# Optimization experiments

Hardware: AMD Instinct MI355X
Metric: run time of the kernel (lower is better)

## Reference

```python
import jax, jax.numpy as jnp
import numpy as np

D_MODEL = 1024
NUM_HEAD = 16
D_K = D_MODEL // NUM_HEAD
FFN_D = 4096
EPS = 1e-5


def _layernorm(x, gamma, beta):
    mu = jnp.mean(x, axis=-1, keepdims=True)
    var = jnp.mean(jnp.square(x - mu), axis=-1, keepdims=True)
    return (x - mu) * jax.lax.rsqrt(var + EPS) * gamma + beta


def setup_inputs() -> dict:
    key = jax.random.key(0)
    ks = jax.random.split(key, 16)
    s = 1.0 / np.sqrt(D_MODEL)
    sf = 1.0 / np.sqrt(FFN_D)
    # weights stored as [in, out] (transpose of torch nn.Linear.weight)
    return {
        "x": jax.random.normal(ks[0], (4, 2048, D_MODEL), dtype=jnp.float32),
        "wq": jax.random.uniform(ks[1], (D_MODEL, D_MODEL), jnp.float32, -s, s),
        "bq": jax.random.uniform(ks[2], (D_MODEL,), jnp.float32, -s, s),
        "wk": jax.random.uniform(ks[3], (D_MODEL, D_MODEL), jnp.float32, -s, s),
        "bk": jax.random.uniform(ks[4], (D_MODEL,), jnp.float32, -s, s),
        "wv": jax.random.uniform(ks[5], (D_MODEL, D_MODEL), jnp.float32, -s, s),
        "bv": jax.random.uniform(ks[6], (D_MODEL,), jnp.float32, -s, s),
        "wo": jax.random.uniform(ks[7], (D_MODEL, D_MODEL), jnp.float32, -s, s),
        "bo": jax.random.uniform(ks[8], (D_MODEL,), jnp.float32, -s, s),
        "w1": jax.random.uniform(ks[9], (D_MODEL, FFN_D), jnp.float32, -s, s),
        "b1": jax.random.uniform(ks[10], (FFN_D,), jnp.float32, -s, s),
        "w2": jax.random.uniform(ks[11], (FFN_D, D_MODEL), jnp.float32, -sf, sf),
        "b2": jax.random.uniform(ks[12], (D_MODEL,), jnp.float32, -sf, sf),
        "g1": jnp.ones((D_MODEL,), jnp.float32),
        "be1": jnp.zeros((D_MODEL,), jnp.float32),
        "g2": jnp.ones((D_MODEL,), jnp.float32),
        "be2": jnp.zeros((D_MODEL,), jnp.float32),
    }


def reference(x, wq, bq, wk, bk, wv, bv, wo, bo, w1, b1, w2, b2, g1, be1, g2, be2):
    B, S, _ = x.shape
    resid1 = x
    # project and split heads: [B, H, S, d_k]
    def heads(w, b):
        return (x @ w + b).reshape(B, S, NUM_HEAD, D_K).transpose(0, 2, 1, 3)
    q = heads(wq, bq)
    k = heads(wk, bk)
    v = heads(wv, bv)
    scores = jnp.einsum("bhsd,bhtd->bhst", q, k) / jnp.sqrt(jnp.float32(D_K))
    attn = jax.nn.softmax(scores, axis=-1)
    ctx = jnp.einsum("bhst,bhtd->bhsd", attn, v)
    ctx = ctx.transpose(0, 2, 1, 3).reshape(B, S, D_MODEL)
    attn_out = ctx @ wo + bo
    x1 = _layernorm(resid1 + attn_out, g1, be1)
    ffn = jax.nn.relu(x1 @ w1 + b1) @ w2 + b2
    return _layernorm(x1 + ffn, g2, be2)
```

## Files before the change

### kernel.cpp

```cpp
#include <hip/hip_runtime.h>

typedef unsigned short u16;
typedef __attribute__((ext_vector_type(8))) u16 u16x8;
typedef __attribute__((ext_vector_type(8))) __bf16 bf16x8;
typedef __attribute__((ext_vector_type(4))) float floatx4;
typedef __attribute__((ext_vector_type(16))) float floatx16;
typedef __attribute__((ext_vector_type(4))) unsigned int u32x4;

#define MFMA16(a, b, c) __builtin_amdgcn_mfma_f32_16x16x32_bf16( \
    __builtin_bit_cast(bf16x8, a), __builtin_bit_cast(bf16x8, b), c, 0, 0, 0)
#define MFMA32(a, b, c) __builtin_amdgcn_mfma_f32_32x32x16_bf16( \
    __builtin_bit_cast(bf16x8, a), __builtin_bit_cast(bf16x8, b), c, 0, 0, 0)

#if __has_builtin(__builtin_amdgcn_exp2f)
#define EXP2(x) __builtin_amdgcn_exp2f(x)
#else
#define EXP2(x) exp2f(x)
#endif

__device__ __forceinline__ float bf2f(u16 h) {
  unsigned u = ((unsigned)h) << 16;
  float f;
  __builtin_memcpy(&f, &u, 4);
  return f;
}
__device__ __forceinline__ u16 f2bf(float f) {
  unsigned u;
  __builtin_memcpy(&u, &f, 4);
  u += 0x7fff + ((u >> 16) & 1);
  return (u16)(u >> 16);
}

__device__ __forceinline__ unsigned cvt_pk_bf16(float a, float b) {
  unsigned r;
  asm("v_cvt_pk_bf16_f32 %0, %1, %2" : "=v"(r) : "v"(a), "v"(b));
  return r;
}
__device__ __forceinline__ void pl32_swap(unsigned& a, unsigned& b) {
  asm("v_permlane32_swap_b32 %0, %1" : "+v"(a), "+v"(b));
}

typedef __attribute__((address_space(1))) const unsigned int gas_u32;
typedef __attribute__((address_space(3))) unsigned int las_u32;

__device__ __forceinline__ void gld_lds16(const u16* g, u16* l) {
  __builtin_amdgcn_global_load_lds((gas_u32*)g, (las_u32*)l, 16, 0, 0);
}

__global__ __launch_bounds__(256) void transpose_k(const float* __restrict__ in,
                                                   u16* __restrict__ out, int R, int C) {
  __shared__ u16 tile[64][65];
  int c0 = blockIdx.x * 64, r0 = blockIdx.y * 64;
  int tc = threadIdx.x & 63, tr = threadIdx.x >> 6;
#pragma unroll
  for (int i = 0; i < 16; ++i)
    tile[tr + i * 4][tc] = f2bf(in[(size_t)(r0 + tr + i * 4) * C + c0 + tc]);
  __syncthreads();
#pragma unroll
  for (int i = 0; i < 16; ++i)
    out[(size_t)(c0 + tr + i * 4) * R + r0 + tc] = tile[tc][tr + i * 4];
}

__global__ __launch_bounds__(256) void convert_k(const float* __restrict__ in,
                                                 u16* __restrict__ out) {
  size_t idx = ((size_t)blockIdx.x * 256 + threadIdx.x) * 8;
  floatx4 f0 = *(const floatx4*)(in + idx);
  floatx4 f1 = *(const floatx4*)(in + idx + 4);
  u16x8 o;
#pragma unroll
  for (int e = 0; e < 4; ++e) o[e] = f2bf(f0[e]);
#pragma unroll
  for (int e = 0; e < 4; ++e) o[4 + e] = f2bf(f1[e]);
  *(u16x8*)(out + idx) = o;
}

template <bool C_F32, bool BIAS_ROW>
__global__ __launch_bounds__(256, 2) void gemm_bt(const u16* __restrict__ A,
                                                  const u16* __restrict__ BT,
                                                  const float* __restrict__ bias,
                                                  void* __restrict__ Cv, int M, int N, int K,
                                                  int relu) {
  __shared__ __align__(16) u16 As[128 * 32];
  __shared__ __align__(16) u16 Bs[128 * 32];
  const int tid = threadIdx.x, lane = tid & 63, wave = tid >> 6;
  const int quad = lane >> 4, l15 = lane & 15;
  const int wr = wave >> 1, wc = wave & 1;
  const int m0 = blockIdx.x * 128, n0 = blockIdx.y * 128;

  floatx4 acc[4][4] = {};

  for (int k0 = 0; k0 < K; k0 += 32) {
#pragma unroll
    for (int p = 0; p < 2; ++p) {
      int chunk = p * 256 + tid;
      int row = chunk >> 2, cc = chunk & 3;
      int ldsbase = (p * 256 + wave * 64) * 8;
      gld_lds16(A + (size_t)(m0 + row) * K + k0 + cc * 8, As + ldsbase);
      gld_lds16(BT + (size_t)(n0 + row) * K + k0 + cc * 8, Bs + ldsbase);
    }
    __syncthreads();
    u16x8 af[4], bfr[4];
#pragma unroll
    for (int i = 0; i < 4; ++i)
      af[i] = *(const u16x8*)(As + (wr * 64 + i * 16 + l15) * 32 + quad * 8);
#pragma unroll
    for (int j = 0; j < 4; ++j)
      bfr[j] = *(const u16x8*)(Bs + (wc * 64 + j * 16 + l15) * 32 + quad * 8);
#pragma unroll
    for (int i = 0; i < 4; ++i)
#pragma unroll
      for (int j = 0; j < 4; ++j) acc[i][j] = MFMA16(af[i], bfr[j], acc[i][j]);
    __syncthreads();
  }

#pragma unroll
  for (int j = 0; j < 4; ++j) {
    int col = n0 + wc * 64 + j * 16 + l15;
    float bv = BIAS_ROW ? 0.f : bias[col];
#pragma unroll
    for (int i = 0; i < 4; ++i) {
      int row = m0 + wr * 64 + i * 16 + quad * 4;
#pragma unroll
      for (int r = 0; r < 4; ++r) {
        float v = acc[i][j][r] + (BIAS_ROW ? bias[row + r] : bv);
        if (relu) v = fmaxf(v, 0.f);
        if (C_F32)
          ((float*)Cv)[(size_t)(row + r) * N + col] = v;
        else
          ((u16*)Cv)[(size_t)(row + r) * N + col] = f2bf(v);
      }
    }
  }
}

__global__ __launch_bounds__(256, 4) void attn_k(const u16* __restrict__ Q,
                                                 const u16* __restrict__ Km,
                                                 const u16* __restrict__ Vt,
                                                 u16* __restrict__ O) {
  __shared__ __align__(16) u16 sh[16384];
  const int tid = threadIdx.x, lane = tid & 63, w = tid >> 6;
  const int hi = lane >> 5, l31 = lane & 31;
  const int b = blockIdx.z, h = blockIdx.y, q0 = blockIdx.x * 128;
  const size_t tokbase = (size_t)b * 2048;

#pragma unroll
  for (int p = 0; p < 4; ++p) {
    int chunk = p * 256 + tid, row = chunk >> 3, cc = chunk & 7;
    int gc = cc ^ (row & 7);
    gld_lds16(Q + (tokbase + q0 + row) * 1024 + h * 64 + gc * 8, sh + (p * 256 + w * 64) * 8);
  }
  __syncthreads();
  u16x8 qf[4];
#pragma unroll
  for (int kt = 0; kt < 4; ++kt) {
    int r = w * 32 + l31;
    int sel = (kt * 2 + hi) ^ (r & 7);
    u16x8 t = *(const u16x8*)(sh + r * 64 + sel * 8);
#pragma unroll
    for (int e = 0; e < 8; ++e) t[e] = f2bf(bf2f(t[e]) * 0.18033688011f);
    qf[kt] = t;
  }
  __syncthreads();

  floatx16 oacc0 = {}, oacc1 = {};
  float lsum = 0.f;

  auto stage = [&](int it2, int buf) {
    int t0 = it2 * 64;
#pragma unroll
    for (int p = 0; p < 2; ++p) {
      int chunk = p * 256 + tid;
      int row = chunk >> 3, cc = chunk & 7;
      int gc = cc ^ (row & 7);
      int ldsoff = (p * 256 + w * 64) * 8;
      gld_lds16(Km + (tokbase + t0 + row) * 1024 + h * 64 + gc * 8, sh + buf * 4096 + ldsoff);
      gld_lds16(Vt + ((size_t)(h * 64 + row)) * 8192 + tokbase + t0 + gc * 8,
                sh + 8192 + buf * 4096 + ldsoff);
    }
  };

  stage(0, 0);

  for (int it = 0; it < 32; ++it) {
    const int cur = it & 1;
    __syncthreads();
    if (it + 1 < 32) stage(it + 1, cur ^ 1);
    const u16* kb = sh + cur * 4096;
    const u16* vb = sh + 8192 + cur * 4096;

    u32x4 pf[4];
#pragma unroll
    for (int tt = 0; tt < 2; ++tt) {
      u16x8 ka[4];
#pragma unroll
      for (int kt = 0; kt < 4; ++kt) {
        int r = tt * 32 + l31;
        ka[kt] = *(const u16x8*)(kb + r * 64 + (((kt * 2 + hi) ^ (r & 7)) * 8));
      }
      floatx16 s = {};
      __builtin_amdgcn_s_setprio(1);
#pragma unroll
      for (int kt = 0; kt < 4; ++kt) s = MFMA32(ka[kt], qf[kt], s);
      __builtin_amdgcn_s_setprio(0);

      float p[16];
#pragma unroll
      for (int r = 0; r < 16; ++r) p[r] = EXP2(s[r]);
#pragma unroll
      for (int r = 0; r < 16; ++r) lsum += p[r];
#pragma unroll
      for (int half = 0; half < 2; ++half) {
        unsigned X0 = cvt_pk_bf16(p[half * 8 + 0], p[half * 8 + 1]);
        unsigned X1 = cvt_pk_bf16(p[half * 8 + 2], p[half * 8 + 3]);
        unsigned Y0 = cvt_pk_bf16(p[half * 8 + 4], p[half * 8 + 5]);
        unsigned Y1 = cvt_pk_bf16(p[half * 8 + 6], p[half * 8 + 7]);
        pl32_swap(X0, Y0);
        pl32_swap(X1, Y1);
        u32x4 f;
        f[0] = X0; f[1] = X1; f[2] = Y0; f[3] = Y1;
        pf[tt * 2 + half] = f;
      }
    }

    {
      u16x8 va[4];
#pragma unroll
      for (int kt = 0; kt < 4; ++kt) {
        int r = l31;
        va[kt] = *(const u16x8*)(vb + r * 64 + (((kt * 2 + hi) ^ (r & 7)) * 8));
      }
      __builtin_amdgcn_s_setprio(1);
#pragma unroll
      for (int kt = 0; kt < 4; ++kt)
        oacc0 = MFMA32(va[kt], __builtin_bit_cast(u16x8, pf[kt]), oacc0);
      __builtin_amdgcn_s_setprio(0);
#pragma unroll
      for (int kt = 0; kt < 4; ++kt) {
        int r = 32 + l31;
        va[kt] = *(const u16x8*)(vb + r * 64 + (((kt * 2 + hi) ^ (r & 7)) * 8));
      }
      __builtin_amdgcn_s_setprio(1);
#pragma unroll
      for (int kt = 0; kt < 4; ++kt)
        oacc1 = MFMA32(va[kt], __builtin_bit_cast(u16x8, pf[kt]), oacc1);
      __builtin_amdgcn_s_setprio(0);
    }
  }

  __syncthreads();
  float tot = lsum + __shfl_xor(lsum, 32);
  float inv = 1.0f / fmaxf(tot, 1e-30f);
  const int qrow = w * 32 + l31;
#pragma unroll
  for (int dt = 0; dt < 2; ++dt) {
    const floatx16& oa = dt ? oacc1 : oacc0;
#pragma unroll
    for (int pr = 0; pr < 8; ++pr) {
      float a = oa[2 * pr] * inv, bb = oa[2 * pr + 1] * inv;
      unsigned pkw = (unsigned)f2bf(a) | ((unsigned)f2bf(bb) << 16);
      int d = dt * 32 + (pr & 1) * 2 + (pr >> 1) * 8 + 4 * hi;
      *(unsigned*)(sh + qrow * 72 + d) = pkw;
    }
  }
  __syncthreads();
#pragma unroll
  for (int p2 = 0; p2 < 4; ++p2) {
    int c = p2 * 64 + lane, rl = c >> 3, cc = c & 7;
    u16x8 vv = *(const u16x8*)(sh + (w * 32 + rl) * 72 + cc * 8);
    *(u16x8*)(O + (tokbase + q0 + w * 32 + rl) * 1024 + h * 64 + cc * 8) = vv;
  }
}

template <bool A_F32, bool B_F32, bool OUT_F32>
__global__ __launch_bounds__(256) void ln_k(const void* __restrict__ Av,
                                            const void* __restrict__ Bv,
                                            const float* __restrict__ g,
                                            const float* __restrict__ be,
                                            void* __restrict__ outv) {
  const int lane = threadIdx.x & 63, wave = threadIdx.x >> 6;
  const size_t row = (size_t)blockIdx.x * 4 + wave;
  const size_t base = row * 1024 + lane * 16;
  float v[16];
  if (A_F32) {
    const float* a = (const float*)Av + base;
#pragma unroll
    for (int q = 0; q < 4; ++q) {
      floatx4 t = *(const floatx4*)(a + q * 4);
#pragma unroll
      for (int e = 0; e < 4; ++e) v[q * 4 + e] = t[e];
    }
  } else {
    const u16* a = (const u16*)Av + base;
    u16x8 a0 = *(const u16x8*)a, a1 = *(const u16x8*)(a + 8);
#pragma unroll
    for (int e = 0; e < 8; ++e) {
      v[e] = bf2f(a0[e]);
      v[e + 8] = bf2f(a1[e]);
    }
  }
  if (B_F32) {
    const float* bb = (const float*)Bv + base;
#pragma unroll
    for (int q = 0; q < 4; ++q) {
      floatx4 t = *(const floatx4*)(bb + q * 4);
#pragma unroll
      for (int e = 0; e < 4; ++e) v[q * 4 + e] += t[e];
    }
  } else {
    const u16* bb = (const u16*)Bv + base;
    u16x8 b0 = *(const u16x8*)bb, b1 = *(const u16x8*)(bb + 8);
#pragma unroll
    for (int e = 0; e < 8; ++e) {
      v[e] += bf2f(b0[e]);
      v[e + 8] += bf2f(b1[e]);
    }
  }
  float sum = 0.f, sq = 0.f;
#pragma unroll
  for (int e = 0; e < 16; ++e) {
    sum += v[e];
    sq += v[e] * v[e];
  }
#pragma unroll
  for (int mk = 1; mk < 64; mk <<= 1) {
    sum += __shfl_xor(sum, mk);
    sq += __shfl_xor(sq, mk);
  }
  float mu = sum * (1.f / 1024.f);
  float var = fmaxf(sq * (1.f / 1024.f) - mu * mu, 0.f);
  float rstd = rsqrtf(var + 1e-5f);
  if (OUT_F32) {
    float* o = (float*)outv + base;
#pragma unroll
    for (int q = 0; q < 4; ++q) {
      floatx4 t;
#pragma unroll
      for (int e = 0; e < 4; ++e) {
        int c = lane * 16 + q * 4 + e;
        t[e] = (v[q * 4 + e] - mu) * rstd * g[c] + be[c];
      }
      *(floatx4*)(o + q * 4) = t;
    }
  } else {
    u16x8 o0, o1;
#pragma unroll
    for (int e = 0; e < 8; ++e) {
      int c = lane * 16 + e;
      o0[e] = f2bf((v[e] - mu) * rstd * g[c] + be[c]);
      o1[e] = f2bf((v[e + 8] - mu) * rstd * g[c + 8] + be[c + 8]);
    }
    *(u16x8*)((u16*)outv + base) = o0;
    *(u16x8*)((u16*)outv + base + 8) = o1;
  }
}

extern "C" void kernel_launch(void* const* d_in, const int* in_sizes, int n_in, void* d_out,
                              int out_size, void* d_ws, size_t ws_size, hipStream_t stream) {
  const float* x = (const float*)d_in[0];
  const float* wq = (const float*)d_in[1];
  const float* bq = (const float*)d_in[2];
  const float* wk = (const float*)d_in[3];
  const float* bk = (const float*)d_in[4];
  const float* wv = (const float*)d_in[5];
  const float* bv = (const float*)d_in[6];
  const float* wo = (const float*)d_in[7];
  const float* bo = (const float*)d_in[8];
  const float* w1 = (const float*)d_in[9];
  const float* b1 = (const float*)d_in[10];
  const float* w2 = (const float*)d_in[11];
  const float* b2 = (const float*)d_in[12];
  const float* g1 = (const float*)d_in[13];
  const float* be1 = (const float*)d_in[14];
  const float* g2 = (const float*)d_in[15];
  const float* be2 = (const float*)d_in[16];
  float* out = (float*)d_out;

  u16* W = (u16*)d_ws;
  const size_t M1 = (size_t)1 << 20;
  u16* wqT = W;
  u16* wkT = wqT + M1;
  u16* wvT = wkT + M1;
  u16* woT = wvT + M1;
  u16* w1T = woT + M1;
  u16* w2T = w1T + 4 * M1;
  u16* arena = w2T + 4 * M1;
  const size_t S8M = (size_t)8 << 20;
  u16* xb = arena;
  u16* Qb = arena + S8M;
  u16* Kb = arena + 2 * S8M;
  u16* Vtb = arena + 3 * S8M;
  u16* Cb = arena + 4 * S8M;
  u16* AO = Qb;
  u16* X1 = xb;
  u16* F1 = Qb;

  dim3 blk(256);
  transpose_k<<<dim3(16, 16), blk, 0, stream>>>(wq, wqT, 1024, 1024);
  transpose_k<<<dim3(16, 16), blk, 0, stream>>>(wk, wkT, 1024, 1024);
  transpose_k<<<dim3(16, 16), blk, 0, stream>>>(wv, wvT, 1024, 1024);
  transpose_k<<<dim3(16, 16), blk, 0, stream>>>(wo, woT, 1024, 1024);
  transpose_k<<<dim3(64, 16), blk, 0, stream>>>(w1, w1T, 1024, 4096);
  transpose_k<<<dim3(16, 64), blk, 0, stream>>>(w2, w2T, 4096, 1024);
  convert_k<<<4096, blk, 0, stream>>>(x, xb);

  gemm_bt<false, false><<<dim3(64, 8), blk, 0, stream>>>(xb, wqT, bq, Qb, 8192, 1024, 1024, 0);
  gemm_bt<false, false><<<dim3(64, 8), blk, 0, stream>>>(xb, wkT, bk, Kb, 8192, 1024, 1024, 0);
  gemm_bt<false, true><<<dim3(8, 64), blk, 0, stream>>>(wvT, xb, bv, Vtb, 1024, 8192, 1024, 0);

  attn_k<<<dim3(16, 16, 4), blk, 0, stream>>>(Qb, Kb, Vtb, Cb);

  gemm_bt<false, false><<<dim3(64, 8), blk, 0, stream>>>(Cb, woT, bo, AO, 8192, 1024, 1024, 0);
  ln_k<true, false, false><<<2048, blk, 0, stream>>>(x, AO, g1, be1, X1);

  gemm_bt<false, false><<<dim3(64, 32), blk, 0, stream>>>(X1, w1T, b1, F1, 8192, 4096, 1024, 1);
  gemm_bt<true, false><<<dim3(64, 8), blk, 0, stream>>>(F1, w2T, b2, out, 8192, 1024, 4096, 0);
  ln_k<false, true, true><<<2048, blk, 0, stream>>>(X1, out, g2, be2, out);
}
```

Measured before the change: 575.7 us.

## Double-buffer GEMM LDS tiles with BK=64 and XOR-swizzled layout

The bf16 GEMM kernel now uses two LDS buffers with a 64-wide K tile. The loads for the next tile are issued right after a single barrier, so they overlap the MFMA work on the current tile, and the second barrier per iteration is gone. Tile columns are XOR-swizzled by row to cut LDS bank conflicts on the fragment reads. LDS use per block rises to 64KB, which could limit occupancy, and the barrier's implicit wait on outstanding loads may limit how much overlap is actually achieved.

```diff
diff --git a/kernel.cpp b/kernel.cpp
--- a/kernel.cpp
+++ b/kernel.cpp
@@ -80,8 +80,8 @@
                                                   const float* __restrict__ bias,
                                                   void* __restrict__ Cv, int M, int N, int K,
                                                   int relu) {
-  __shared__ __align__(16) u16 As[128 * 32];
-  __shared__ __align__(16) u16 Bs[128 * 32];
+  __shared__ __align__(16) u16 As[2][128 * 64];
+  __shared__ __align__(16) u16 Bs[2][128 * 64];
   const int tid = threadIdx.x, lane = tid & 63, wave = tid >> 6;
   const int quad = lane >> 4, l15 = lane & 15;
   const int wr = wave >> 1, wc = wave & 1;
@@ -89,28 +89,45 @@
 
   floatx4 acc[4][4] = {};
 
-  for (int k0 = 0; k0 < K; k0 += 32) {
-#pragma unroll
-    for (int p = 0; p < 2; ++p) {
+  auto stage = [&](int kt, int buf) {
+    int k0 = kt * 64;
+#pragma unroll
+    for (int p = 0; p < 4; ++p) {
       int chunk = p * 256 + tid;
-      int row = chunk >> 2, cc = chunk & 3;
-      int ldsbase = (p * 256 + wave * 64) * 8;
-      gld_lds16(A + (size_t)(m0 + row) * K + k0 + cc * 8, As + ldsbase);
-      gld_lds16(BT + (size_t)(n0 + row) * K + k0 + cc * 8, Bs + ldsbase);
-    }
+      int row = chunk >> 3, cc = chunk & 7;
+      int gc = cc ^ (row & 7);
+      int ldsoff = (p * 256 + wave * 64) * 8;
+      gld_lds16(A + (size_t)(m0 + row) * K + k0 + gc * 8, &As[buf][ldsoff]);
+      gld_lds16(BT + (size_t)(n0 + row) * K + k0 + gc * 8, &Bs[buf][ldsoff]);
+    }
+  };
+
+  const int nk = K >> 6;
+  stage(0, 0);
+
+  for (int kt = 0; kt < nk; ++kt) {
+    const int cur = kt & 1;
     __syncthreads();
-    u16x8 af[4], bfr[4];
-#pragma unroll
-    for (int i = 0; i < 4; ++i)
-      af[i] = *(const u16x8*)(As + (wr * 64 + i * 16 + l15) * 32 + quad * 8);
-#pragma unroll
-    for (int j = 0; j < 4; ++j)
-      bfr[j] = *(const u16x8*)(Bs + (wc * 64 + j * 16 + l15) * 32 + quad * 8);
-#pragma unroll
-    for (int i = 0; i < 4; ++i)
-#pragma unroll
-      for (int j = 0; j < 4; ++j) acc[i][j] = MFMA16(af[i], bfr[j], acc[i][j]);
-    __syncthreads();
+    if (kt + 1 < nk) stage(kt + 1, cur ^ 1);
+
+#pragma unroll
+    for (int ks = 0; ks < 2; ++ks) {
+      u16x8 af[4], bfr[4];
+#pragma unroll
+      for (int i = 0; i < 4; ++i) {
+        int r = wr * 64 + i * 16 + l15;
+        af[i] = *(const u16x8*)(&As[cur][r * 64 + (((ks * 4 + quad) ^ (r & 7)) * 8)]);
+      }
+#pragma unroll
+      for (int j = 0; j < 4; ++j) {
+        int r = wc * 64 + j * 16 + l15;
+        bfr[j] = *(const u16x8*)(&Bs[cur][r * 64 + (((ks * 4 + quad) ^ (r & 7)) * 8)]);
+      }
+#pragma unroll
+      for (int i = 0; i < 4; ++i)
+#pragma unroll
+        for (int j = 0; j < 4; ++j) acc[i][j] = MFMA16(af[i], bfr[j], acc[i][j]);
+    }
   }
 
 #pragma unroll
```

After: 528.2 us. 8.2% less time.
